# Optimization experiments

Hardware: AMD Instinct MI355X
Metric: run time of the kernel (lower is better)

## Reference

```python
import jax, jax.numpy as jnp
import numpy as np

N = 100000   # nodes per graph (50k users + 50k items)
E = 1600000  # edges per graph
D = 128      # feature / hidden dim
B = 100000   # train pairs per domain
NUM_USER = 50000
LAMBDA = 1.0


def setup_inputs() -> dict:
    key = jax.random.key(0)
    ks = jax.random.split(key, 24)
    s = 1.0 / np.sqrt(D)
    return {
        "feats_s": jax.random.normal(ks[0], (N, D), jnp.float32),
        "feats_t": jax.random.normal(ks[1], (N, D), jnp.float32),
        "W1": jax.random.normal(ks[2], (D, D), jnp.float32) * s,
        "b1": jnp.zeros((D,), jnp.float32),
        "W2": jax.random.normal(ks[3], (D, D), jnp.float32) * s,
        "b2": jnp.zeros((D,), jnp.float32),
        "cls_W": jax.random.normal(ks[4], (2 * D, 1), jnp.float32) * s,
        "cls_b": jnp.zeros((1,), jnp.float32),
        "du_W": jax.random.normal(ks[5], (D, 1), jnp.float32) * s,
        "du_b": jnp.zeros((1,), jnp.float32),
        "di_W": jax.random.normal(ks[6], (D, 1), jnp.float32) * s,
        "di_b": jnp.zeros((1,), jnp.float32),
        "edge_src_s": jax.random.randint(ks[7], (E,), 0, N, jnp.int32),
        "edge_dst_s": jax.random.randint(ks[8], (E,), 0, N, jnp.int32),
        "edge_src_t": jax.random.randint(ks[9], (E,), 0, N, jnp.int32),
        "edge_dst_t": jax.random.randint(ks[10], (E,), 0, N, jnp.int32),
        "user_s": jax.random.randint(ks[11], (B,), 0, NUM_USER, jnp.int32),
        "item_s": jax.random.randint(ks[12], (B,), 0, NUM_USER, jnp.int32),
        "labels_s": jax.random.randint(ks[13], (B,), 0, 2, jnp.int32),
        "user_t": jax.random.randint(ks[14], (B,), 0, NUM_USER, jnp.int32),
        "item_t": jax.random.randint(ks[15], (B,), 0, NUM_USER, jnp.int32),
        "labels_t": jax.random.randint(ks[16], (B,), 0, 2, jnp.int32),
        "num_user_ds": NUM_USER,
        "num_user_dt": NUM_USER,
    }


def _gcn_layer(x, W, b, src, dst, dinv):
    # PyG GCNConv: out[i] = sum_{j->i} dinv[j]*dinv[i] * (x @ W)[j] + b
    h = x @ W
    norm = (dinv[src] * dinv[dst])[:, None]
    return jax.ops.segment_sum(h[src] * norm, dst, num_segments=x.shape[0]) + b


def _encode(x, src, dst, W1, b1, W2, b2):
    n = x.shape[0]
    sl = jnp.arange(n, dtype=src.dtype)            # self loops
    src = jnp.concatenate([src, sl])
    dst = jnp.concatenate([dst, sl])
    deg = jax.ops.segment_sum(jnp.ones_like(dst, dtype=x.dtype), dst, num_segments=n)
    dinv = jax.lax.rsqrt(jnp.maximum(deg, 1.0))    # deg >= 1 due to self loops
    h = jax.nn.relu(_gcn_layer(x, W1, b1, src, dst, dinv))
    return _gcn_layer(h, W2, b2, src, dst, dinv)   # dropout is identity at eval


def _bce_from_logits(z, y):
    # mean BCE on sigmoid(z), numerically stable
    return jnp.mean(y * jax.nn.softplus(-z) + (1.0 - y) * jax.nn.softplus(z))


def reference(feats_s, feats_t, W1, b1, W2, b2, cls_W, cls_b, du_W, du_b, di_W, di_b,
              edge_src_s, edge_dst_s, edge_src_t, edge_dst_t,
              user_s, item_s, labels_s, user_t, item_t, labels_t,
              num_user_ds, num_user_dt):
    x_ds = _encode(feats_s, edge_src_s, edge_dst_s, W1, b1, W2, b2)
    x_dt = _encode(feats_t, edge_src_t, edge_dst_t, W1, b1, W2, b2)

    ufs = x_ds[user_s]
    ifs = x_ds[item_s + num_user_ds]
    uft = x_dt[user_t]
    ift = x_dt[item_t + num_user_dt]

    z_s = (jnp.concatenate([ufs, ifs], axis=1) @ cls_W).reshape(-1) + cls_b[0]
    z_t = (jnp.concatenate([uft, ift], axis=1) @ cls_W).reshape(-1) + cls_b[0]
    clf_loss = _bce_from_logits(z_s, labels_s.astype(jnp.float32)) + \
               _bce_from_logits(z_t, labels_t.astype(jnp.float32))

    cu_s = jax.nn.sigmoid((ufs @ du_W).reshape(-1) + du_b[0])
    cu_t = jax.nn.sigmoid((uft @ du_W).reshape(-1) + du_b[0])
    ci_s = jax.nn.sigmoid((ifs @ di_W).reshape(-1) + di_b[0])
    ci_t = jax.nn.sigmoid((ift @ di_W).reshape(-1) + di_b[0])
    domain_loss = jnp.abs(jnp.mean(cu_s) - jnp.mean(cu_t)) + \
                  jnp.abs(jnp.mean(ci_s) - jnp.mean(ci_t))

    return clf_loss + LAMBDA * domain_loss
```

## Files before the change

### kernel.cpp

```cpp
#include <hip/hip_runtime.h>

#define D 128
#define NB 512
#define BSLACK 4112

typedef __attribute__((ext_vector_type(8))) short bf16x8;
typedef __attribute__((ext_vector_type(4))) float f32x4;
typedef __attribute__((ext_vector_type(2))) float f32x2;

static __device__ inline unsigned pack_bf16x2(float a, float b) {
    unsigned ua = __float_as_uint(a);
    unsigned ub = __float_as_uint(b);
    ua += 0x7fffu + ((ua >> 16) & 1u);
    ub += 0x7fffu + ((ub >> 16) & 1u);
    return (ua >> 16) | (ub & 0xffff0000u);
}

__global__ __launch_bounds__(256) void bh_k(const int* __restrict__ dst_s,
                                            const int* __restrict__ dst_t,
                                            int* __restrict__ bcnt, int E) {
    int d = blockIdx.y;
    const int* dst = d ? dst_t : dst_s;
    __shared__ int h[NB];
    for (int i = threadIdx.x; i < NB; i += 256) h[i] = 0;
    __syncthreads();
    int stride = gridDim.x * 256;
    for (int e = blockIdx.x * 256 + threadIdx.x; e < E; e += stride)
        atomicAdd(&h[dst[e] >> 8], 1);
    __syncthreads();
    for (int i = threadIdx.x; i < NB; i += 256)
        if (h[i]) atomicAdd(&bcnt[d * NB + i], h[i]);
}

__global__ __launch_bounds__(1024) void scanB_k(const int* __restrict__ bcnt,
                                                int* __restrict__ bbase,
                                                int* __restrict__ cursor) {
    __shared__ int sh[1024];
    int t = threadIdx.x;
    int v = bcnt[t];
    sh[t] = v;
    __syncthreads();
    for (int o = 1; o < 1024; o <<= 1) {
        int x = (t >= o) ? sh[t - o] : 0;
        __syncthreads();
        sh[t] += x;
        __syncthreads();
    }
    int ex = sh[t] - v;
    bbase[t] = ex; cursor[t] = ex;
    if (t == 1023) bbase[1024] = sh[1023];
}

__global__ __launch_bounds__(256) void bin_k(const int* __restrict__ src_s,
                                             const int* __restrict__ dst_s,
                                             const int* __restrict__ src_t,
                                             const int* __restrict__ dst_t,
                                             int* __restrict__ cursor,
                                             unsigned* __restrict__ pairs, int E) {
    int d = blockIdx.y;
    const int* src = d ? src_t : src_s;
    const int* dst = d ? dst_t : dst_s;
    int* cur = cursor + d * NB;
    __shared__ int h[NB];
    __shared__ int gb[NB];
    int t0 = blockIdx.x * 2048;
    if (t0 >= E) return;
    for (int i = threadIdx.x; i < NB; i += 256) h[i] = 0;
    __syncthreads();
    int rank[8]; unsigned pk[8]; short bk[8];
    #pragma unroll
    for (int j = 0; j < 8; ++j) {
        int e = t0 + j * 256 + threadIdx.x;
        if (e < E) {
            int dd = dst[e], s = src[e];
            bk[j] = (short)(dd >> 8);
            pk[j] = (unsigned)s | ((unsigned)(dd & 255) << 24);
            rank[j] = atomicAdd(&h[dd >> 8], 1);
        } else bk[j] = -1;
    }
    __syncthreads();
    for (int i = threadIdx.x; i < NB; i += 256)
        gb[i] = h[i] ? atomicAdd(&cur[i], h[i]) : 0;
    __syncthreads();
    #pragma unroll
    for (int j = 0; j < 8; ++j)
        if (bk[j] >= 0) pairs[gb[bk[j]] + rank[j]] = pk[j];
}

__global__ __launch_bounds__(256) void csrb_k(const unsigned* __restrict__ pairs,
                                              const int* __restrict__ bbase,
                                              int2* __restrict__ nspan,
                                              float* __restrict__ dinv,
                                              int* __restrict__ csr, int N) {
    int d = blockIdx.y, bx = blockIdx.x, t = threadIdx.x;
    int g = d * NB + bx;
    int e0 = bbase[g], e1 = bbase[g + 1];
    int cbase = ((e0 + 15) & ~15) + g * BSLACK;
    float* dv = dinv + (size_t)d * (N + 1);
    int2* ns = nspan + (size_t)d * N;
    __shared__ int lh[256];
    __shared__ int lex[256];
    __shared__ int lc[256];
    lh[t] = 0; lc[t] = 0;
    __syncthreads();
    for (int e = e0 + t; e < e1; e += 256)
        atomicAdd(&lh[pairs[e] >> 24], 1);
    __syncthreads();
    int node = (bx << 8) + t;
    bool valid = node < N;
    int deg = lh[t];
    int pdeg = valid ? (((deg + 16) >> 4) << 4) : 0;
    lex[t] = pdeg;
    __syncthreads();
    for (int o = 1; o < 256; o <<= 1) {
        int x = (t >= o) ? lex[t - o] : 0;
        __syncthreads();
        lex[t] += x;
        __syncthreads();
    }
    int start = cbase + lex[t] - pdeg;
    if (valid) {
        ns[node] = make_int2(start, start + pdeg);
        dv[node] = rsqrtf((float)(deg + 1));
    }
    lex[t] = start;
    __syncthreads();
    for (int e = e0 + t; e < e1; e += 256) {
        unsigned p = pairs[e];
        int dn = p >> 24;
        int rank = atomicAdd(&lc[dn], 1);
        csr[lex[dn] + rank] = (int)(p & 0xffffffu);
    }
    __syncthreads();
    if (valid) {
        int b = lex[t];
        csr[b + deg] = node;
        for (int k = deg + 1; k < pdeg; ++k) csr[b + k] = N;
    }
    if (bx == 0 && t == 0) dv[N] = 0.f;
}

__global__ __launch_bounds__(256) void packW_k(const float* __restrict__ W1,
                                               const float* __restrict__ W2,
                                               unsigned short* __restrict__ wp1,
                                               unsigned short* __restrict__ wp2) {
    const float* W = blockIdx.x ? W2 : W1;
    unsigned short* wp = blockIdx.x ? wp2 : wp1;
    for (int idx = threadIdx.x; idx < 2048; idx += 256) {
        int f = idx >> 6, lane = idx & 63;
        int t = f >> 2, c = f & 3;
        int q = lane >> 4, nn = lane & 15;
        #pragma unroll
        for (int j = 0; j < 8; ++j) {
            unsigned u = __float_as_uint(W[(c * 32 + q * 8 + j) * 128 + t * 16 + nn]);
            u += 0x7fffu + ((u >> 16) & 1u);
            wp[idx * 8 + j] = (unsigned short)(u >> 16);
        }
    }
}

__global__ __launch_bounds__(256) void gemm_mfma(const void* __restrict__ xs,
                                                 const void* __restrict__ xt,
                                                 const unsigned short* __restrict__ wp,
                                                 unsigned* __restrict__ hb,
                                                 const float* __restrict__ dinv,
                                                 int N, int in_bf16) {
    int d = blockIdx.y;
    const void* xin = d ? xt : xs;
    unsigned* out = hb + (size_t)d * (N + 1) * 32;
    const float* dv = dinv + (size_t)d * (N + 1);
    __shared__ float cs[64 * 132];
    int tid = threadIdx.x;
    int wave = tid >> 6, lane = tid & 63;
    int quad = lane >> 4, nn = lane & 15;
    long long blockbase = (long long)blockIdx.x * 64;
    long long ar = blockbase + wave * 16 + nn;
    if (ar > N - 1) ar = N - 1;

    bf16x8 a[4];
    if (in_bf16) {
        const uint4* xr = (const uint4*)((const unsigned short*)xin + ar * 128);
        #pragma unroll
        for (int c = 0; c < 4; ++c) {
            union { uint4 u; bf16x8 v; } cv;
            cv.u = xr[c * 4 + quad];
            a[c] = cv.v;
        }
    } else {
        const float4* xr = (const float4*)((const float*)xin + ar * 128);
        #pragma unroll
        for (int c = 0; c < 4; ++c) {
            float4 lo = xr[c * 8 + quad * 2];
            float4 hi = xr[c * 8 + quad * 2 + 1];
            union { bf16x8 v; unsigned u[4]; } au;
            au.u[0] = pack_bf16x2(lo.x, lo.y);
            au.u[1] = pack_bf16x2(lo.z, lo.w);
            au.u[2] = pack_bf16x2(hi.x, hi.y);
            au.u[3] = pack_bf16x2(hi.z, hi.w);
            a[c] = au.v;
        }
    }

    f32x4 acc[8];
    #pragma unroll
    for (int t = 0; t < 8; ++t) acc[t] = (f32x4){0.f, 0.f, 0.f, 0.f};
    const bf16x8* wf = (const bf16x8*)wp;
    #pragma unroll
    for (int t = 0; t < 8; ++t) {
        #pragma unroll
        for (int c = 0; c < 4; ++c) {
            bf16x8 b = wf[(t * 4 + c) * 64 + lane];
            acc[t] = __builtin_amdgcn_mfma_f32_16x16x32_bf16(a[c], b, acc[t], 0, 0, 0);
        }
    }

    #pragma unroll
    for (int t = 0; t < 8; ++t) {
        #pragma unroll
        for (int r = 0; r < 4; ++r)
            cs[(wave * 16 + quad * 4 + r) * 132 + t * 16 + nn] = acc[t][r];
    }
    __syncthreads();

    #pragma unroll
    for (int i = 0; i < 8; ++i) {
        int idx = tid + i * 256;
        int r = idx >> 5, c4 = idx & 31;
        long long row = blockbase + r;
        if (row <= N) {
            float s = dv[row];
            const float4 v = *(const float4*)&cs[r * 132 + c4 * 4];
            int pk = __builtin_amdgcn_cvt_pk_fp8_f32(v.x * s, v.y * s, 0, false);
            pk = __builtin_amdgcn_cvt_pk_fp8_f32(v.z * s, v.w * s, pk, true);
            out[row * 32 + c4] = (unsigned)pk;
        }
    }
}

#define AGG_BODY(hs, sp)                                                        \
    float a0 = 0.f, a1 = 0.f, a2 = 0.f, a3 = 0.f;                               \
    {                                                                           \
        int e = sp.x;                                                           \
        const int* cp = csr + 8 * half;                                         \
        int4 c0 = *(const int4*)(cp + e);                                       \
        int4 c1 = *(const int4*)(cp + e + 4);                                   \
        for (;;) {                                                              \
            int4 p0 = c0, p1 = c1;                                              \
            int en = e + 16;                                                    \
            c0 = *(const int4*)(cp + en);            \
            c1 = *(const int4*)(cp + en + 4);                                   \
            unsigned u0 = hs[((unsigned)p0.x << 5) | li];                       \
            unsigned u1 = hs[((unsigned)p0.y << 5) | li];                       \
            unsigned u2 = hs[((unsigned)p0.z << 5) | li];                       \
            unsigned u3 = hs[((unsigned)p0.w << 5) | li];                       \
            unsigned u4 = hs[((unsigned)p1.x << 5) | li];                       \
            unsigned u5 = hs[((unsigned)p1.y << 5) | li];                       \
            unsigned u6 = hs[((unsigned)p1.z << 5) | li];                       \
            unsigned u7 = hs[((unsigned)p1.w << 5) | li];                       \
            f32x2 lo, hi;                                                       \
            lo = __builtin_amdgcn_cvt_pk_f32_fp8((int)u0, false);               \
            hi = __builtin_amdgcn_cvt_pk_f32_fp8((int)u0, true);                \
            a0 += lo[0]; a1 += lo[1]; a2 += hi[0]; a3 += hi[1];                 \
            lo = __builtin_amdgcn_cvt_pk_f32_fp8((int)u1, false);               \
            hi = __builtin_amdgcn_cvt_pk_f32_fp8((int)u1, true);                \
            a0 += lo[0]; a1 += lo[1]; a2 += hi[0]; a3 += hi[1];                 \
            lo = __builtin_amdgcn_cvt_pk_f32_fp8((int)u2, false);               \
            hi = __builtin_amdgcn_cvt_pk_f32_fp8((int)u2, true);                \
            a0 += lo[0]; a1 += lo[1]; a2 += hi[0]; a3 += hi[1];                 \
            lo = __builtin_amdgcn_cvt_pk_f32_fp8((int)u3, false);               \
            hi = __builtin_amdgcn_cvt_pk_f32_fp8((int)u3, true);                \
            a0 += lo[0]; a1 += lo[1]; a2 += hi[0]; a3 += hi[1];                 \
            lo = __builtin_amdgcn_cvt_pk_f32_fp8((int)u4, false);               \
            hi = __builtin_amdgcn_cvt_pk_f32_fp8((int)u4, true);                \
            a0 += lo[0]; a1 += lo[1]; a2 += hi[0]; a3 += hi[1];                 \
            lo = __builtin_amdgcn_cvt_pk_f32_fp8((int)u5, false);               \
            hi = __builtin_amdgcn_cvt_pk_f32_fp8((int)u5, true);                \
            a0 += lo[0]; a1 += lo[1]; a2 += hi[0]; a3 += hi[1];                 \
            lo = __builtin_amdgcn_cvt_pk_f32_fp8((int)u6, false);               \
            hi = __builtin_amdgcn_cvt_pk_f32_fp8((int)u6, true);                \
            a0 += lo[0]; a1 += lo[1]; a2 += hi[0]; a3 += hi[1];                 \
            lo = __builtin_amdgcn_cvt_pk_f32_fp8((int)u7, false);               \
            hi = __builtin_amdgcn_cvt_pk_f32_fp8((int)u7, true);                \
            a0 += lo[0]; a1 += lo[1]; a2 += hi[0]; a3 += hi[1];                 \
            if (en >= sp.y) break;                                              \
            e = en;                                                             \
        }                                                                       \
    }                                                                           \
    a0 += __shfl_xor(a0, 32);                                                   \
    a1 += __shfl_xor(a1, 32);                                                   \
    a2 += __shfl_xor(a2, 32);                                                   \
    a3 += __shfl_xor(a3, 32);

__global__ __launch_bounds__(256) void agg1_k(const unsigned* __restrict__ hb,
                                              const float* __restrict__ dinv,
                                              const int2* __restrict__ nspan,
                                              const int* __restrict__ csr,
                                              const float* __restrict__ bias,
                                              uint2* __restrict__ abuf, int N) {
    int d = blockIdx.y;
    const unsigned* hs = hb + (size_t)d * (N + 1) * 32;
    const float* dv = dinv + (size_t)d * (N + 1);
    const int2* ns = nspan + (size_t)d * N;
    uint2* out = abuf + (size_t)d * N * 32;
    int wave = threadIdx.x >> 6, lane = threadIdx.x & 63;
    int node = blockIdx.x * 4 + wave;
    if (node >= N) return;
    int half = lane >> 5, li = lane & 31;
    int2 sp = ns[node];
    AGG_BODY(hs, sp)
    if (half == 0) {
        float di = dv[node];
        float4 b4 = ((const float4*)bias)[li];
        float o0 = fmaxf(fmaf(di, a0, b4.x), 0.f);
        float o1 = fmaxf(fmaf(di, a1, b4.y), 0.f);
        float o2 = fmaxf(fmaf(di, a2, b4.z), 0.f);
        float o3 = fmaxf(fmaf(di, a3, b4.w), 0.f);
        out[(size_t)node * 32 + li] = make_uint2(pack_bf16x2(o0, o1), pack_bf16x2(o2, o3));
    }
}

__global__ __launch_bounds__(256) void agg2_k(const unsigned* __restrict__ hb,
                                              const float* __restrict__ dinv,
                                              const int2* __restrict__ nspan,
                                              const int* __restrict__ csr,
                                              const float* __restrict__ bias,
                                              const float* __restrict__ clsW,
                                              const float* __restrict__ duW,
                                              const float* __restrict__ diW,
                                              const int* __restrict__ nus,
                                              const int* __restrict__ nut,
                                              float2* __restrict__ nodeDots, int N) {
    int d = blockIdx.y;
    const unsigned* hs = hb + (size_t)d * (N + 1) * 32;
    const float* dv = dinv + (size_t)d * (N + 1);
    const int2* ns = nspan + (size_t)d * N;
    float2* nd = nodeDots + (size_t)d * N;
    int nu = d ? nut[0] : nus[0];
    int wave = threadIdx.x >> 6, lane = threadIdx.x & 63;
    int node = blockIdx.x * 4 + wave;
    if (node >= N) return;
    int half = lane >> 5, li = lane & 31;
    int2 sp = ns[node];
    AGG_BODY(hs, sp)
    float di = dv[node];
    float4 b4 = ((const float4*)bias)[li];
    float o0 = fmaf(di, a0, b4.x);
    float o1 = fmaf(di, a1, b4.y);
    float o2 = fmaf(di, a2, b4.z);
    float o3 = fmaf(di, a3, b4.w);
    int sel = (node >= nu) ? 1 : 0;
    float4 wA = ((const float4*)clsW)[sel * 32 + li];
    float4 wB = ((const float4*)(sel ? diW : duW))[li];
    float p = o0 * wA.x + o1 * wA.y + o2 * wA.z + o3 * wA.w;
    float q = o0 * wB.x + o1 * wB.y + o2 * wB.z + o3 * wB.w;
    #pragma unroll
    for (int o = 16; o > 0; o >>= 1) {
        p += __shfl_xor(p, o);
        q += __shfl_xor(q, o);
    }
    if (lane == 0) nd[node] = make_float2(p, q);
}

__global__ __launch_bounds__(256) void loss_k(const float2* __restrict__ nodeDots,
                                              const int* __restrict__ us, const int* __restrict__ is_,
                                              const int* __restrict__ ls,
                                              const int* __restrict__ ut, const int* __restrict__ it,
                                              const int* __restrict__ lt,
                                              const float* __restrict__ clsb,
                                              const float* __restrict__ dub,
                                              const float* __restrict__ dib,
                                              const int* __restrict__ nus,
                                              const int* __restrict__ nut,
                                              float* __restrict__ accum, int Bn, int N) {
    int d = blockIdx.y;
    const float2* nd = nodeDots + (size_t)d * N;
    const int* users = d ? ut : us;
    const int* items = d ? it : is_;
    const int* labels = d ? lt : ls;
    int nu = d ? nut[0] : nus[0];
    float* acc = accum + 3 * d;
    int k = blockIdx.x * 256 + threadIdx.x;
    float bce = 0.f, cu = 0.f, ci = 0.f;
    if (k < Bn) {
        int u = users[k];
        int t = items[k] + nu;
        float2 ud = nd[u];
        float2 id = nd[t];
        float z = ud.x + id.x + clsb[0];
        float y = (float)labels[k];
        float sp = fmaxf(z, 0.f) + log1pf(expf(-fabsf(z)));
        bce = sp - y * z;
        cu = 1.f / (1.f + expf(-(ud.y + dub[0])));
        ci = 1.f / (1.f + expf(-(id.y + dib[0])));
    }
    #pragma unroll
    for (int o = 32; o > 0; o >>= 1) {
        bce += __shfl_xor(bce, o);
        cu += __shfl_xor(cu, o);
        ci += __shfl_xor(ci, o);
    }
    __shared__ float sh[12];
    int lane = threadIdx.x & 63, wave = threadIdx.x >> 6;
    if (lane == 0) { sh[wave * 3 + 0] = bce; sh[wave * 3 + 1] = cu; sh[wave * 3 + 2] = ci; }
    __syncthreads();
    if (threadIdx.x < 3) {
        float v = sh[threadIdx.x] + sh[3 + threadIdx.x] + sh[6 + threadIdx.x] + sh[9 + threadIdx.x];
        atomicAdd(&acc[threadIdx.x], v);
    }
}

__global__ void finalize_k(const float* __restrict__ accum, float* __restrict__ out, float invB) {
    if (threadIdx.x == 0 && blockIdx.x == 0) {
        float clf = (accum[0] + accum[3]) * invB;
        float dom = fabsf((accum[1] - accum[4]) * invB) + fabsf((accum[2] - accum[5]) * invB);
        out[0] = clf + dom;
    }
}

extern "C" void kernel_launch(void* const* d_in, const int* in_sizes, int n_in,
                              void* d_out, int out_size, void* d_ws, size_t ws_size,
                              hipStream_t stream) {
    const float* feats_s = (const float*)d_in[0];
    const float* feats_t = (const float*)d_in[1];
    const float* W1   = (const float*)d_in[2];
    const float* b1   = (const float*)d_in[3];
    const float* W2   = (const float*)d_in[4];
    const float* b2   = (const float*)d_in[5];
    const float* clsW = (const float*)d_in[6];
    const float* clsb = (const float*)d_in[7];
    const float* duW  = (const float*)d_in[8];
    const float* dub  = (const float*)d_in[9];
    const float* diW  = (const float*)d_in[10];
    const float* dib  = (const float*)d_in[11];

    int N = in_sizes[0] / D;
    int E = in_sizes[12];
    int B = in_sizes[16];
    int nb = (N + 255) >> 8;

    char* ws = (char*)d_ws;
    size_t off = 0;
    auto alloc = [&](size_t bytes) -> void* {
        void* p = ws + off;
        off += (bytes + 255) & ~(size_t)255;
        return p;
    };
    int*      bcnt   = (int*)  alloc(2 * NB * 4);
    int*      bbase  = (int*)  alloc((2 * NB + 1) * 4);
    int*      cursor = (int*)  alloc(2 * NB * 4);
    float*    dinv   = (float*)alloc((size_t)2 * (N + 1) * 4);
    int2*     nspan  = (int2*) alloc((size_t)2 * N * 8);
    unsigned* pairs  = (unsigned*)alloc((size_t)2 * E * 4);
    int*      csr    = (int*)  alloc(((size_t)2 * E + 2 * NB * BSLACK + 256) * 4);
    unsigned* hbuf8  = (unsigned*)alloc((size_t)2 * (N + 1) * 128);
    unsigned* abuf   = (unsigned*)alloc((size_t)2 * N * 256);
    float2*   nodeDots = (float2*)alloc((size_t)2 * N * 8);
    unsigned short* wp1 = (unsigned short*)alloc(16384 * 2);
    unsigned short* wp2 = (unsigned short*)alloc(16384 * 2);
    float*    accum  = (float*)alloc(128);

    hipMemsetAsync(accum, 0, 6 * sizeof(float), stream);
    hipMemsetAsync(bcnt, 0, 2 * NB * 4, stream);

    const int* esrc_s = (const int*)d_in[12];
    const int* edst_s = (const int*)d_in[13];
    const int* esrc_t = (const int*)d_in[14];
    const int* edst_t = (const int*)d_in[15];
    const int* user_s = (const int*)d_in[16];
    const int* item_s = (const int*)d_in[17];
    const int* lab_s  = (const int*)d_in[18];
    const int* user_t = (const int*)d_in[19];
    const int* item_t = (const int*)d_in[20];
    const int* lab_t  = (const int*)d_in[21];
    const int* nup_s  = (const int*)d_in[22];
    const int* nup_t  = (const int*)d_in[23];

    packW_k<<<2, 256, 0, stream>>>(W1, W2, wp1, wp2);

    bh_k<<<dim3(512, 2), 256, 0, stream>>>(edst_s, edst_t, bcnt, E);
    scanB_k<<<1, 1024, 0, stream>>>(bcnt, bbase, cursor);
    bin_k<<<dim3((E + 2047) / 2048, 2), 256, 0, stream>>>(esrc_s, edst_s, esrc_t, edst_t,
                                                          cursor, pairs, E);
    csrb_k<<<dim3(nb, 2), 256, 0, stream>>>(pairs, bbase, nspan, dinv, csr, N);

    int ngb = (N + 64) / 64;
    gemm_mfma<<<dim3(ngb, 2), 256, 0, stream>>>(feats_s, feats_t, wp1, hbuf8, dinv, N, 0);
    agg1_k<<<dim3((N + 3) / 4, 2), 256, 0, stream>>>(hbuf8, dinv, nspan, csr, b1,
                                                     (uint2*)abuf, N);
    gemm_mfma<<<dim3(ngb, 2), 256, 0, stream>>>(abuf, abuf + (size_t)N * 64, wp2,
                                                hbuf8, dinv, N, 1);
    agg2_k<<<dim3((N + 3) / 4, 2), 256, 0, stream>>>(hbuf8, dinv, nspan, csr, b2,
                                                     clsW, duW, diW, nup_s, nup_t,
                                                     nodeDots, N);
    loss_k<<<dim3((B + 255) / 256, 2), 256, 0, stream>>>(nodeDots,
                                                         user_s, item_s, lab_s,
                                                         user_t, item_t, lab_t,
                                                         clsb, dub, dib, nup_s, nup_t,
                                                         accum, B, N);
    finalize_k<<<1, 64, 0, stream>>>(accum, (float*)d_out, 1.0f / (float)B);
}
```

Measured before the change: 493.0 us.

## Process chunks of eight nodes per wave in aggregation kernels with streaming CSR

```diff
diff --git a/kernel.cpp b/kernel.cpp
--- a/kernel.cpp
+++ b/kernel.cpp
@@ -3,10 +3,12 @@
 #define D 128
 #define NB 512
 #define BSLACK 4112
+#define CHUNK 8
 
 typedef __attribute__((ext_vector_type(8))) short bf16x8;
 typedef __attribute__((ext_vector_type(4))) float f32x4;
 typedef __attribute__((ext_vector_type(2))) float f32x2;
+typedef __attribute__((ext_vector_type(4))) int i32x4;
 
 static __device__ inline unsigned pack_bf16x2(float a, float b) {
     unsigned ua = __float_as_uint(a);
@@ -237,59 +239,40 @@
     }
 }
 
-#define AGG_BODY(hs, sp)                                                        \
-    float a0 = 0.f, a1 = 0.f, a2 = 0.f, a3 = 0.f;                               \
-    {                                                                           \
-        int e = sp.x;                                                           \
-        const int* cp = csr + 8 * half;                                         \
-        int4 c0 = *(const int4*)(cp + e);                                       \
-        int4 c1 = *(const int4*)(cp + e + 4);                                   \
-        for (;;) {                                                              \
-            int4 p0 = c0, p1 = c1;                                              \
-            int en = e + 16;                                                    \
-            c0 = *(const int4*)(cp + en);            \
-            c1 = *(const int4*)(cp + en + 4);                                   \
-            unsigned u0 = hs[((unsigned)p0.x << 5) | li];                       \
-            unsigned u1 = hs[((unsigned)p0.y << 5) | li];                       \
-            unsigned u2 = hs[((unsigned)p0.z << 5) | li];                       \
-            unsigned u3 = hs[((unsigned)p0.w << 5) | li];                       \
-            unsigned u4 = hs[((unsigned)p1.x << 5) | li];                       \
-            unsigned u5 = hs[((unsigned)p1.y << 5) | li];                       \
-            unsigned u6 = hs[((unsigned)p1.z << 5) | li];                       \
-            unsigned u7 = hs[((unsigned)p1.w << 5) | li];                       \
-            f32x2 lo, hi;                                                       \
-            lo = __builtin_amdgcn_cvt_pk_f32_fp8((int)u0, false);               \
-            hi = __builtin_amdgcn_cvt_pk_f32_fp8((int)u0, true);                \
-            a0 += lo[0]; a1 += lo[1]; a2 += hi[0]; a3 += hi[1];                 \
-            lo = __builtin_amdgcn_cvt_pk_f32_fp8((int)u1, false);               \
-            hi = __builtin_amdgcn_cvt_pk_f32_fp8((int)u1, true);                \
-            a0 += lo[0]; a1 += lo[1]; a2 += hi[0]; a3 += hi[1];                 \
-            lo = __builtin_amdgcn_cvt_pk_f32_fp8((int)u2, false);               \
-            hi = __builtin_amdgcn_cvt_pk_f32_fp8((int)u2, true);                \
-            a0 += lo[0]; a1 += lo[1]; a2 += hi[0]; a3 += hi[1];                 \
-            lo = __builtin_amdgcn_cvt_pk_f32_fp8((int)u3, false);               \
-            hi = __builtin_amdgcn_cvt_pk_f32_fp8((int)u3, true);                \
-            a0 += lo[0]; a1 += lo[1]; a2 += hi[0]; a3 += hi[1];                 \
-            lo = __builtin_amdgcn_cvt_pk_f32_fp8((int)u4, false);               \
-            hi = __builtin_amdgcn_cvt_pk_f32_fp8((int)u4, true);                \
-            a0 += lo[0]; a1 += lo[1]; a2 += hi[0]; a3 += hi[1];                 \
-            lo = __builtin_amdgcn_cvt_pk_f32_fp8((int)u5, false);               \
-            hi = __builtin_amdgcn_cvt_pk_f32_fp8((int)u5, true);                \
-            a0 += lo[0]; a1 += lo[1]; a2 += hi[0]; a3 += hi[1];                 \
-            lo = __builtin_amdgcn_cvt_pk_f32_fp8((int)u6, false);               \
-            hi = __builtin_amdgcn_cvt_pk_f32_fp8((int)u6, true);                \
-            a0 += lo[0]; a1 += lo[1]; a2 += hi[0]; a3 += hi[1];                 \
-            lo = __builtin_amdgcn_cvt_pk_f32_fp8((int)u7, false);               \
-            hi = __builtin_amdgcn_cvt_pk_f32_fp8((int)u7, true);                \
-            a0 += lo[0]; a1 += lo[1]; a2 += hi[0]; a3 += hi[1];                 \
-            if (en >= sp.y) break;                                              \
-            e = en;                                                             \
-        }                                                                       \
-    }                                                                           \
-    a0 += __shfl_xor(a0, 32);                                                   \
-    a1 += __shfl_xor(a1, 32);                                                   \
-    a2 += __shfl_xor(a2, 32);                                                   \
-    a3 += __shfl_xor(a3, 32);
+#define AGG_WINDOW(hsl, p0, p1)                                                 \
+        unsigned u0 = hsl[(unsigned)p0.x << 5];                                 \
+        unsigned u1 = hsl[(unsigned)p0.y << 5];                                 \
+        unsigned u2 = hsl[(unsigned)p0.z << 5];                                 \
+        unsigned u3 = hsl[(unsigned)p0.w << 5];                                 \
+        unsigned u4 = hsl[(unsigned)p1.x << 5];                                 \
+        unsigned u5 = hsl[(unsigned)p1.y << 5];                                 \
+        unsigned u6 = hsl[(unsigned)p1.z << 5];                                 \
+        unsigned u7 = hsl[(unsigned)p1.w << 5];                                 \
+        f32x2 lo, hi;                                                           \
+        lo = __builtin_amdgcn_cvt_pk_f32_fp8((int)u0, false);                   \
+        hi = __builtin_amdgcn_cvt_pk_f32_fp8((int)u0, true);                    \
+        s01 += lo; s23 += hi;                                                   \
+        lo = __builtin_amdgcn_cvt_pk_f32_fp8((int)u1, false);                   \
+        hi = __builtin_amdgcn_cvt_pk_f32_fp8((int)u1, true);                    \
+        s01 += lo; s23 += hi;                                                   \
+        lo = __builtin_amdgcn_cvt_pk_f32_fp8((int)u2, false);                   \
+        hi = __builtin_amdgcn_cvt_pk_f32_fp8((int)u2, true);                    \
+        s01 += lo; s23 += hi;                                                   \
+        lo = __builtin_amdgcn_cvt_pk_f32_fp8((int)u3, false);                   \
+        hi = __builtin_amdgcn_cvt_pk_f32_fp8((int)u3, true);                    \
+        s01 += lo; s23 += hi;                                                   \
+        lo = __builtin_amdgcn_cvt_pk_f32_fp8((int)u4, false);                   \
+        hi = __builtin_amdgcn_cvt_pk_f32_fp8((int)u4, true);                    \
+        s01 += lo; s23 += hi;                                                   \
+        lo = __builtin_amdgcn_cvt_pk_f32_fp8((int)u5, false);                   \
+        hi = __builtin_amdgcn_cvt_pk_f32_fp8((int)u5, true);                    \
+        s01 += lo; s23 += hi;                                                   \
+        lo = __builtin_amdgcn_cvt_pk_f32_fp8((int)u6, false);                   \
+        hi = __builtin_amdgcn_cvt_pk_f32_fp8((int)u6, true);                    \
+        s01 += lo; s23 += hi;                                                   \
+        lo = __builtin_amdgcn_cvt_pk_f32_fp8((int)u7, false);                   \
+        hi = __builtin_amdgcn_cvt_pk_f32_fp8((int)u7, true);                    \
+        s01 += lo; s23 += hi;
 
 __global__ __launch_bounds__(256) void agg1_k(const unsigned* __restrict__ hb,
                                               const float* __restrict__ dinv,
@@ -303,19 +286,51 @@
     const int2* ns = nspan + (size_t)d * N;
     uint2* out = abuf + (size_t)d * N * 32;
     int wave = threadIdx.x >> 6, lane = threadIdx.x & 63;
-    int node = blockIdx.x * 4 + wave;
-    if (node >= N) return;
+    int node0 = (blockIdx.x * 4 + wave) * CHUNK;
+    if (node0 >= N) return;
+    int cnt = min(CHUNK, N - node0);
     int half = lane >> 5, li = lane & 31;
-    int2 sp = ns[node];
-    AGG_BODY(hs, sp)
-    if (half == 0) {
-        float di = dv[node];
-        float4 b4 = ((const float4*)bias)[li];
-        float o0 = fmaxf(fmaf(di, a0, b4.x), 0.f);
-        float o1 = fmaxf(fmaf(di, a1, b4.y), 0.f);
-        float o2 = fmaxf(fmaf(di, a2, b4.z), 0.f);
-        float o3 = fmaxf(fmaf(di, a3, b4.w), 0.f);
-        out[(size_t)node * 32 + li] = make_uint2(pack_bf16x2(o0, o1), pack_bf16x2(o2, o3));
+    int lc = lane & (CHUNK - 1);
+    int2 myns = make_int2(0, 0);
+    float mydv = 0.f;
+    if (lc < cnt) { myns = ns[node0 + lc]; mydv = dv[node0 + lc]; }
+    float4 b4 = ((const float4*)bias)[li];
+    const unsigned* hsl = hs + li;
+    const int* cp = csr + 8 * half;
+
+    int k = 0;
+    int e = __shfl(myns.x, 0);
+    int end = __shfl(myns.y, 0);
+    f32x2 s01 = (f32x2){0.f, 0.f};
+    f32x2 s23 = (f32x2){0.f, 0.f};
+    i32x4 c0 = __builtin_nontemporal_load((const i32x4*)(cp + e));
+    i32x4 c1 = __builtin_nontemporal_load((const i32x4*)(cp + e + 4));
+    for (;;) {
+        i32x4 p0 = c0, p1 = c1;
+        int en = e + 16;
+        c0 = __builtin_nontemporal_load((const i32x4*)(cp + en));
+        c1 = __builtin_nontemporal_load((const i32x4*)(cp + en + 4));
+        AGG_WINDOW(hsl, p0, p1)
+        if (en >= end) {
+            float a0 = s01[0], a1 = s01[1], a2 = s23[0], a3 = s23[1];
+            a0 += __shfl_xor(a0, 32);
+            a1 += __shfl_xor(a1, 32);
+            a2 += __shfl_xor(a2, 32);
+            a3 += __shfl_xor(a3, 32);
+            float dik = __shfl(mydv, k);
+            float o0 = fmaxf(fmaf(dik, a0, b4.x), 0.f);
+            float o1 = fmaxf(fmaf(dik, a1, b4.y), 0.f);
+            float o2 = fmaxf(fmaf(dik, a2, b4.z), 0.f);
+            float o3 = fmaxf(fmaf(dik, a3, b4.w), 0.f);
+            if (half == 0)
+                out[(size_t)(node0 + k) * 32 + li] =
+                    make_uint2(pack_bf16x2(o0, o1), pack_bf16x2(o2, o3));
+            if (++k >= cnt) break;
+            end = __shfl(myns.y, k);
+            s01 = (f32x2){0.f, 0.f};
+            s23 = (f32x2){0.f, 0.f};
+        }
+        e = en;
     }
 }
 
@@ -337,28 +352,65 @@
     float2* nd = nodeDots + (size_t)d * N;
     int nu = d ? nut[0] : nus[0];
     int wave = threadIdx.x >> 6, lane = threadIdx.x & 63;
-    int node = blockIdx.x * 4 + wave;
-    if (node >= N) return;
+    int node0 = (blockIdx.x * 4 + wave) * CHUNK;
+    if (node0 >= N) return;
+    int cnt = min(CHUNK, N - node0);
     int half = lane >> 5, li = lane & 31;
-    int2 sp = ns[node];
-    AGG_BODY(hs, sp)
-    float di = dv[node];
+    int lc = lane & (CHUNK - 1);
+    int2 myns = make_int2(0, 0);
+    float mydv = 0.f;
+    if (lc < cnt) { myns = ns[node0 + lc]; mydv = dv[node0 + lc]; }
     float4 b4 = ((const float4*)bias)[li];
-    float o0 = fmaf(di, a0, b4.x);
-    float o1 = fmaf(di, a1, b4.y);
-    float o2 = fmaf(di, a2, b4.z);
-    float o3 = fmaf(di, a3, b4.w);
-    int sel = (node >= nu) ? 1 : 0;
-    float4 wA = ((const float4*)clsW)[sel * 32 + li];
-    float4 wB = ((const float4*)(sel ? diW : duW))[li];
-    float p = o0 * wA.x + o1 * wA.y + o2 * wA.z + o3 * wA.w;
-    float q = o0 * wB.x + o1 * wB.y + o2 * wB.z + o3 * wB.w;
-    #pragma unroll
-    for (int o = 16; o > 0; o >>= 1) {
-        p += __shfl_xor(p, o);
-        q += __shfl_xor(q, o);
-    }
-    if (lane == 0) nd[node] = make_float2(p, q);
+    float4 wA0 = ((const float4*)clsW)[li];
+    float4 wA1 = ((const float4*)clsW)[32 + li];
+    float4 wB0 = ((const float4*)duW)[li];
+    float4 wB1 = ((const float4*)diW)[li];
+    const unsigned* hsl = hs + li;
+    const int* cp = csr + 8 * half;
+
+    int k = 0;
+    int e = __shfl(myns.x, 0);
+    int end = __shfl(myns.y, 0);
+    f32x2 s01 = (f32x2){0.f, 0.f};
+    f32x2 s23 = (f32x2){0.f, 0.f};
+    i32x4 c0 = __builtin_nontemporal_load((const i32x4*)(cp + e));
+    i32x4 c1 = __builtin_nontemporal_load((const i32x4*)(cp + e + 4));
+    for (;;) {
+        i32x4 p0 = c0, p1 = c1;
+        int en = e + 16;
+        c0 = __builtin_nontemporal_load((const i32x4*)(cp + en));
+        c1 = __builtin_nontemporal_load((const i32x4*)(cp + en + 4));
+        AGG_WINDOW(hsl, p0, p1)
+        if (en >= end) {
+            float a0 = s01[0], a1 = s01[1], a2 = s23[0], a3 = s23[1];
+            a0 += __shfl_xor(a0, 32);
+            a1 += __shfl_xor(a1, 32);
+            a2 += __shfl_xor(a2, 32);
+            a3 += __shfl_xor(a3, 32);
+            float dik = __shfl(mydv, k);
+            float o0 = fmaf(dik, a0, b4.x);
+            float o1 = fmaf(dik, a1, b4.y);
+            float o2 = fmaf(dik, a2, b4.z);
+            float o3 = fmaf(dik, a3, b4.w);
+            int nodek = node0 + k;
+            int sel = (nodek >= nu) ? 1 : 0;
+            float4 wA = sel ? wA1 : wA0;
+            float4 wB = sel ? wB1 : wB0;
+            float p = o0 * wA.x + o1 * wA.y + o2 * wA.z + o3 * wA.w;
+            float q = o0 * wB.x + o1 * wB.y + o2 * wB.z + o3 * wB.w;
+            #pragma unroll
+            for (int o = 16; o > 0; o >>= 1) {
+                p += __shfl_xor(p, o);
+                q += __shfl_xor(q, o);
+            }
+            if (lane == 0) nd[nodek] = make_float2(p, q);
+            if (++k >= cnt) break;
+            end = __shfl(myns.y, k);
+            s01 = (f32x2){0.f, 0.f};
+            s23 = (f32x2){0.f, 0.f};
+        }
+        e = en;
+    }
 }
 
 __global__ __launch_bounds__(256) void loss_k(const float2* __restrict__ nodeDots,
@@ -484,14 +536,15 @@
     csrb_k<<<dim3(nb, 2), 256, 0, stream>>>(pairs, bbase, nspan, dinv, csr, N);
 
     int ngb = (N + 64) / 64;
+    int nchunk = (N + CHUNK - 1) / CHUNK;
     gemm_mfma<<<dim3(ngb, 2), 256, 0, stream>>>(feats_s, feats_t, wp1, hbuf8, dinv, N, 0);
-    agg1_k<<<dim3((N + 3) / 4, 2), 256, 0, stream>>>(hbuf8, dinv, nspan, csr, b1,
-                                                     (uint2*)abuf, N);
+    agg1_k<<<dim3((nchunk + 3) / 4, 2), 256, 0, stream>>>(hbuf8, dinv, nspan, csr, b1,
+                                                          (uint2*)abuf, N);
     gemm_mfma<<<dim3(ngb, 2), 256, 0, stream>>>(abuf, abuf + (size_t)N * 64, wp2,
                                                 hbuf8, dinv, N, 1);
-    agg2_k<<<dim3((N + 3) / 4, 2), 256, 0, stream>>>(hbuf8, dinv, nspan, csr, b2,
-                                                     clsW, duW, diW, nup_s, nup_t,
-                                                     nodeDots, N);
+    agg2_k<<<dim3((nchunk + 3) / 4, 2), 256, 0, stream>>>(hbuf8, dinv, nspan, csr, b2,
+                                                          clsW, duW, diW, nup_s, nup_t,
+                                                          nodeDots, N);
     loss_k<<<dim3((B + 255) / 256, 2), 256, 0, stream>>>(nodeDots,
                                                          user_s, item_s, lab_s,
                                                          user_t, item_t, lab_t,
```

After: 486.7 us. No clear change (-1.3%).
